# Optimization experiments

Measured on AMD Instinct MI355X. Metric: run time of the kernel, lower is better.

## Reference

```python
import jax, jax.numpy as jnp
import numpy as np

N_W, N_E, N_NUC, D_H = 8192, 32, 8, 32


def _init_linear(k, fan_in, fan_out):
    k1, k2 = jax.random.split(k)
    bound = 1.0 / np.sqrt(fan_in)
    W = jax.random.uniform(k1, (fan_in, fan_out), jnp.float32, -bound, bound)
    b = jax.random.uniform(k2, (fan_out,), jnp.float32, -bound, bound)
    return W, b


def setup_inputs() -> dict:
    key = jax.random.key(0)
    ks = jax.random.split(key, 12)
    W1_en, b1_en = _init_linear(ks[4], N_NUC, D_H)
    W2_en, b2_en = _init_linear(ks[5], D_H, D_H)
    W3_en, b3_en = _init_linear(ks[6], D_H, 1)
    W1_ee, b1_ee = _init_linear(ks[7], 1, D_H)
    W2_ee, b2_ee = _init_linear(ks[8], D_H, D_H)
    W3_ee, b3_ee = _init_linear(ks[9], D_H, 1)
    return {
        "r_electrons": jax.random.normal(ks[0], (N_W, N_E, 3), jnp.float32),
        "r_nuclei": jax.random.normal(ks[1], (N_NUC, 3), jnp.float32),
        "charges": jax.random.uniform(ks[2], (N_NUC,), jnp.float32),
        "spin_mask_parallel": jax.random.randint(ks[3], (N_E, N_E), 0, 2).astype(bool),
        "b_en": jnp.ones((N_NUC,), jnp.float32),
        "b_ee": jnp.array(1.0, jnp.float32),
        "W1_en": W1_en, "b1_en": b1_en, "W2_en": W2_en, "b2_en": b2_en,
        "W3_en": W3_en, "b3_en": b3_en,
        "W1_ee": W1_ee, "b1_ee": b1_ee, "W2_ee": W2_ee, "b2_ee": b2_ee,
        "W3_ee": W3_ee, "b3_ee": b3_ee,
        "scale_en": jnp.array(0.1, jnp.float32),
        "scale_ee": jnp.array(0.1, jnp.float32),
    }


def _mlp(x, W1, b1, W2, b2, W3, b3):
    h = jax.nn.silu(x @ W1 + b1)
    h = jax.nn.silu(h @ W2 + b2)
    return h @ W3 + b3


def reference(r_electrons, r_nuclei, charges, spin_mask_parallel,
              b_en, b_ee,
              W1_en, b1_en, W2_en, b2_en, W3_en, b3_en,
              W1_ee, b1_ee, W2_ee, b2_ee, W3_ee, b3_ee,
              scale_en, scale_ee):
    # --- electron-nucleus term ---
    d_en = r_electrons[:, :, None, :] - r_nuclei[None, None, :, :]  # [W,E,Nuc,3]
    r_en = jnp.linalg.norm(d_en, axis=-1)                            # [W,E,Nuc]
    b_en_s = jax.nn.softplus(b_en)
    J_en = jnp.sum(-charges * r_en / (1.0 + b_en_s * r_en), axis=(1, 2))  # [W]
    # r^2-killed neural correction (Linear over nuclei dim)
    J_en_nn = scale_en * jnp.sum(
        _mlp(r_en ** 2, W1_en, b1_en, W2_en, b2_en, W3_en, b3_en)[..., 0], axis=1)
    # --- electron-electron term (upper-triangular pairs only) ---
    iu, ju = np.triu_indices(N_E, k=1)  # static pair index lists, P = E*(E-1)/2
    diff = r_electrons[:, iu, :] - r_electrons[:, ju, :]  # [W,P,3]
    r_ee = jnp.linalg.norm(diff, axis=-1)                  # [W,P]
    a = jnp.where(spin_mask_parallel[iu, ju], 0.25, 0.5)   # [P]
    b_ee_s = jax.nn.softplus(b_ee)
    J_ee = jnp.sum(a * r_ee / (1.0 + b_ee_s * r_ee), axis=1)  # [W]
    J_ee_nn = scale_ee * jnp.sum(
        _mlp(r_ee[..., None], W1_ee, b1_ee, W2_ee, b2_ee, W3_ee, b3_ee)[..., 0], axis=1)
    return J_en + J_en_nn + J_ee + J_ee_nn
```

## Files before the change

kernel.cpp:

```cpp
#include <hip/hip_runtime.h>

#define N_W   8192
#define N_E   32
#define N_NUC 8
#define D_H   32
#define NTAB  4096
#define TAB_INVH 256.0f
#define TAB_H    (1.0f/256.0f)
#define WPB   8

#define AUX_OFF 4096
#define AT_OFF  4112
#define W3S_OFF 4624
#define B_OFF   4656

typedef __attribute__((ext_vector_type(8)))  short bf16x8_t;
typedef __attribute__((ext_vector_type(16))) float f32x16_t;

union FragAB { bf16x8_t s; unsigned u[4]; };

__device__ __forceinline__ float fast_rcp(float x) { return __builtin_amdgcn_rcpf(x); }
__device__ __forceinline__ float silu_f(float v)   { return v * fast_rcp(1.0f + __expf(-v)); }
__device__ __forceinline__ unsigned pk_bf16(float lo, float hi) {
    unsigned r;
    asm("v_cvt_pk_bf16_f32 %0, %1, %2" : "=v"(r) : "v"(lo), "v"(hi));
    return r;
}

__global__ void build_tables(const float* __restrict__ W1ee, const float* __restrict__ b1ee,
                             const float* __restrict__ W2ee, const float* __restrict__ b2ee,
                             const float* __restrict__ W3ee, const float* __restrict__ b3ee,
                             const float* __restrict__ scale_ee,
                             const float* __restrict__ b_en, const float* __restrict__ b_ee,
                             const int* __restrict__ mask,
                             const float* __restrict__ W2en, const float* __restrict__ W3en,
                             const float* __restrict__ b3en, const float* __restrict__ scale_en,
                             float* __restrict__ ws)
{
    const int tid = threadIdx.x;
    if (blockIdx.x == 0) {
        float* aux = ws + AUX_OFF;
        if (tid < N_NUC) aux[tid] = __logf(1.0f + __expf(b_en[tid]));
        if (tid == 8)    aux[8]   = __logf(1.0f + __expf(b_ee[0]));
        if (tid == 9)    aux[9]   = 32.0f * scale_en[0] * b3en[0];
        if (tid < D_H)   ws[W3S_OFF + tid] = W3en[tid] * scale_en[0];
        float* aT = ws + AT_OFF;
#pragma unroll
        for (int q = 0; q < 2; ++q) {
            int idx = tid + q * 256;
            int e = idx >> 4, dm = idx & 15, d = dm + 1;
            int jn = (e + d) & 31;
            int a = e < jn ? e : jn, b = e < jn ? jn : e;
            float av = mask[a * N_E + b] ? 0.25f : 0.5f;
            if (d == 16) av *= 0.5f;
            aT[e * 16 + dm] = av;
        }
        unsigned* wsB = (unsigned*)(ws + B_OFF);
#pragma unroll
        for (int q = 0; q < 2; ++q) {
            int idx = tid + q * 256;
            int lane = idx >> 3, slot = idx & 7;
            int m = slot >> 2, r = slot & 3;
            int k = m * 16 + ((lane >> 5) << 3) + (r << 1);
            int j = lane & 31;
            wsB[lane * 8 + slot] = pk_bf16(W2en[k * D_H + j], W2en[(k + 1) * D_H + j]);
        }
    }
    const int j     = tid & 31;
    const int entry = blockIdx.x * 8 + (tid >> 5);
    const float r   = (float)entry * TAB_H;
    float g = b2ee[j];
#pragma unroll
    for (int k = 0; k < D_H; ++k) g += silu_f(r * W1ee[k] + b1ee[k]) * W2ee[k * D_H + j];
    float o = silu_f(g) * W3ee[j];
#pragma unroll
    for (int m = 16; m; m >>= 1) o += __shfl_xor(o, m, 32);
    if (j == 0) ws[entry] = scale_ee[0] * (o + b3ee[0]);
}

__launch_bounds__(256, 4)
__global__ void jastrow_kernel(const float* __restrict__ re, const float* __restrict__ rnuc,
                               const float* __restrict__ charges,
                               const float* __restrict__ W1, const float* __restrict__ b1,
                               const float* __restrict__ b2,
                               const float* __restrict__ ws,
                               float* __restrict__ out)
{
    const int tid  = threadIdx.x;
    const int e    = tid & 31;
    const int half = (tid >> 5) & 1;
    const int v    = tid >> 5;
    const int w    = blockIdx.x * WPB + v;
    const float* aux = ws + AUX_OFF;

    const float* cb = re + ((size_t)w * N_E + e) * 3;
    float ex = cb[0], ey = cb[1], ez = cb[2];

    float acc = 0.0f;

    float x[N_NUC];
#pragma unroll
    for (int n = 0; n < N_NUC; ++n) {
        float dx = ex - rnuc[n * 3 + 0];
        float dy = ey - rnuc[n * 3 + 1];
        float dz = ez - rnuc[n * 3 + 2];
        float r2 = dx * dx + dy * dy + dz * dz;
        x[n] = r2;
        float r = sqrtf(r2);
        acc -= charges[n] * r * fast_rcp(1.0f + aux[n] * r);
    }

    float2 hh[D_H / 2];
#pragma unroll
    for (int j = 0; j < D_H / 2; ++j) hh[j] = ((const float2*)b1)[j];
#pragma unroll
    for (int k = 0; k < N_NUC; ++k) {
        float xk = x[k];
        const float2* row = (const float2*)(W1 + k * D_H);
#pragma unroll
        for (int j = 0; j < D_H / 2; ++j) {
            float2 wv = row[j];
            hh[j].x = fmaf(xk, wv.x, hh[j].x);
            hh[j].y = fmaf(xk, wv.y, hh[j].y);
        }
    }
    unsigned hpk[16];
#pragma unroll
    for (int i = 0; i < 16; ++i) hpk[i] = pk_bf16(silu_f(hh[i].x), silu_f(hh[i].y));
    unsigned sx[16];
#pragma unroll
    for (int i = 0; i < 16; ++i) sx[i] = (unsigned)__shfl_xor((int)hpk[i], 32, 64);

    FragAB B1, B2;
    {
        const unsigned* wsB = (const unsigned*)(ws + B_OFF) + (size_t)(tid & 63) * 8;
        uint4 q0 = *(const uint4*)wsB;
        uint4 q1 = *(const uint4*)(wsB + 4);
        B1.u[0] = q0.x; B1.u[1] = q0.y; B1.u[2] = q0.z; B1.u[3] = q0.w;
        B2.u[0] = q1.x; B2.u[1] = q1.y; B2.u[2] = q1.z; B2.u[3] = q1.w;
    }
    const bool lo = (tid & 32) == 0;
    FragAB A1a, A2a, A1b, A2b;
#pragma unroll
    for (int r = 0; r < 4; ++r) {
        A1a.u[r] = lo ? hpk[r]      : sx[4 + r];
        A2a.u[r] = lo ? hpk[8 + r]  : sx[12 + r];
        A1b.u[r] = lo ? sx[r]       : hpk[4 + r];
        A2b.u[r] = lo ? sx[8 + r]   : hpk[12 + r];
    }
    float vb2 = b2[e];
    f32x16_t accA, accB;
#pragma unroll
    for (int r = 0; r < 16; ++r) { accA[r] = vb2; accB[r] = vb2; }
    accA = __builtin_amdgcn_mfma_f32_32x32x16_bf16(A1a.s, B1.s, accA, 0, 0, 0);
    accA = __builtin_amdgcn_mfma_f32_32x32x16_bf16(A2a.s, B2.s, accA, 0, 0, 0);
    accB = __builtin_amdgcn_mfma_f32_32x32x16_bf16(A1b.s, B1.s, accB, 0, 0, 0);
    accB = __builtin_amdgcn_mfma_f32_32x32x16_bf16(A2b.s, B2.s, accB, 0, 0, 0);

    float w3s = ws[W3S_OFF + e];
    float sA = 0.0f, sB = 0.0f;
#pragma unroll
    for (int r = 0; r < 16; ++r) { sA += silu_f(accA[r]); sB += silu_f(accB[r]); }
    float mlpA = sA * w3s, mlpB = sB * w3s;

    float bs = aux[8];
    float av[16];
    {
        const float* aT = ws + AT_OFF + e * 16;
#pragma unroll
        for (int i = 0; i < 16; ++i) av[i] = aT[i];
    }
#pragma unroll
    for (int d = 1; d <= 16; ++d) {
        int jn = (e + d) & 31;
        float cjx = __shfl(ex, jn, 32);
        float cjy = __shfl(ey, jn, 32);
        float cjz = __shfl(ez, jn, 32);
        float dx = ex - cjx, dy = ey - cjy, dz = ez - cjz;
        float r = sqrtf(dx * dx + dy * dy + dz * dz);
        float ct = av[d - 1] * r * fast_rcp(1.0f + bs * r);
        float t = r * TAB_INVH;
        int i0 = (int)t;
        if (i0 > NTAB - 2) i0 = NTAB - 2;
        float f = t - (float)i0;
        const float* tp = ws + i0;
        float tv = tp[0] + f * (tp[1] - tp[0]);
        acc += ct + ((d == 16) ? 0.5f * tv : tv);
    }

    float valA = mlpA + (half ? 0.0f : acc);
    float valB = mlpB + (half ? acc : 0.0f);
#pragma unroll
    for (int m = 32; m; m >>= 1) {
        valA += __shfl_xor(valA, m, 64);
        valB += __shfl_xor(valB, m, 64);
    }
    if ((tid & 63) == 0) {
        int wA = blockIdx.x * WPB + ((tid >> 6) << 1);
        out[wA]     = valA + aux[9];
        out[wA + 1] = valB + aux[9];
    }
}

extern "C" void kernel_launch(void* const* d_in, const int* in_sizes, int n_in,
                              void* d_out, int out_size, void* d_ws, size_t ws_size,
                              hipStream_t stream)
{
    const float* re       = (const float*)d_in[0];
    const float* rnuc     = (const float*)d_in[1];
    const float* charges  = (const float*)d_in[2];
    const int*   mask     = (const int*)d_in[3];
    const float* b_en     = (const float*)d_in[4];
    const float* b_ee     = (const float*)d_in[5];
    const float* W1_en    = (const float*)d_in[6];
    const float* b1_en    = (const float*)d_in[7];
    const float* W2_en    = (const float*)d_in[8];
    const float* b2_en    = (const float*)d_in[9];
    const float* W3_en    = (const float*)d_in[10];
    const float* b3_en    = (const float*)d_in[11];
    const float* W1_ee    = (const float*)d_in[12];
    const float* b1_ee    = (const float*)d_in[13];
    const float* W2_ee    = (const float*)d_in[14];
    const float* b2_ee    = (const float*)d_in[15];
    const float* W3_ee    = (const float*)d_in[16];
    const float* b3_ee    = (const float*)d_in[17];
    const float* scale_en = (const float*)d_in[18];
    const float* scale_ee = (const float*)d_in[19];

    float* out = (float*)d_out;
    float* ws  = (float*)d_ws;

    build_tables<<<NTAB / 8, 256, 0, stream>>>(W1_ee, b1_ee, W2_ee, b2_ee, W3_ee, b3_ee,
                                               scale_ee, b_en, b_ee, mask,
                                               W2_en, W3_en, b3_en, scale_en, ws);
    jastrow_kernel<<<N_W / WPB, 256, 0, stream>>>(re, rnuc, charges,
                                                  W1_en, b1_en, b2_en, ws, out);
}
```

Before: 23.49 us.

## Map one walker per wavefront, splitting MLP K-halves and pair loop across half-waves

Restructures the work mapping so each 64-lane wavefront handles a single walker instead of two. Each half-wave now computes its own K-half of the hidden activations, which removes the cross-half shuffles, and a single pair of MFMAs replaces the previous four. The electron-electron pair loop is split between the two half-waves, 8 offsets each. This halves walkers per block and raises the launch-bounds occupancy hint, trading more blocks and duplicated electron-nucleus work for shorter per-thread serial chains.

After: 83.34 us. 255% more time.

```diff
diff --git a/kernel.cpp b/kernel.cpp
--- a/kernel.cpp
+++ b/kernel.cpp
@@ -7,7 +7,7 @@
 #define NTAB  4096
 #define TAB_INVH 256.0f
 #define TAB_H    (1.0f/256.0f)
-#define WPB   8
+#define WPB   4
 
 #define AUX_OFF 4096
 #define AT_OFF  4112
@@ -78,7 +78,7 @@
     if (j == 0) ws[entry] = scale_ee[0] * (o + b3ee[0]);
 }
 
-__launch_bounds__(256, 4)
+__launch_bounds__(256, 8)
 __global__ void jastrow_kernel(const float* __restrict__ re, const float* __restrict__ rnuc,
                                const float* __restrict__ charges,
                                const float* __restrict__ W1, const float* __restrict__ b1,
@@ -86,19 +86,17 @@
                                const float* __restrict__ ws,
                                float* __restrict__ out)
 {
-    const int tid  = threadIdx.x;
-    const int e    = tid & 31;
-    const int half = (tid >> 5) & 1;
-    const int v    = tid >> 5;
-    const int w    = blockIdx.x * WPB + v;
+    const int tid = threadIdx.x;
+    const int e   = tid & 31;
+    const int kh  = (tid >> 5) & 1;
+    const int w   = blockIdx.x * WPB + (tid >> 6);
     const float* aux = ws + AUX_OFF;
 
     const float* cb = re + ((size_t)w * N_E + e) * 3;
     float ex = cb[0], ey = cb[1], ez = cb[2];
 
-    float acc = 0.0f;
-
     float x[N_NUC];
+    float cusp = 0.0f;
 #pragma unroll
     for (int n = 0; n < N_NUC; ++n) {
         float dx = ex - rnuc[n * 3 + 0];
@@ -107,8 +105,9 @@
         float r2 = dx * dx + dy * dy + dz * dz;
         x[n] = r2;
         float r = sqrtf(r2);
-        acc -= charges[n] * r * fast_rcp(1.0f + aux[n] * r);
-    }
+        cusp -= charges[n] * r * fast_rcp(1.0f + aux[n] * r);
+    }
+    float acc = 0.5f * cusp;
 
     float2 hh[D_H / 2];
 #pragma unroll
@@ -124,12 +123,14 @@
             hh[j].y = fmaf(xk, wv.y, hh[j].y);
         }
     }
-    unsigned hpk[16];
-#pragma unroll
-    for (int i = 0; i < 16; ++i) hpk[i] = pk_bf16(silu_f(hh[i].x), silu_f(hh[i].y));
-    unsigned sx[16];
-#pragma unroll
-    for (int i = 0; i < 16; ++i) sx[i] = (unsigned)__shfl_xor((int)hpk[i], 32, 64);
+    FragAB A1, A2;
+#pragma unroll
+    for (int r = 0; r < 4; ++r) {
+        float2 s1 = kh ? hh[4 + r]  : hh[r];
+        float2 s2 = kh ? hh[12 + r] : hh[8 + r];
+        A1.u[r] = pk_bf16(silu_f(s1.x), silu_f(s1.y));
+        A2.u[r] = pk_bf16(silu_f(s2.x), silu_f(s2.y));
+    }
 
     FragAB B1, B2;
     {
@@ -139,67 +140,50 @@
         B1.u[0] = q0.x; B1.u[1] = q0.y; B1.u[2] = q0.z; B1.u[3] = q0.w;
         B2.u[0] = q1.x; B2.u[1] = q1.y; B2.u[2] = q1.z; B2.u[3] = q1.w;
     }
-    const bool lo = (tid & 32) == 0;
-    FragAB A1a, A2a, A1b, A2b;
-#pragma unroll
-    for (int r = 0; r < 4; ++r) {
-        A1a.u[r] = lo ? hpk[r]      : sx[4 + r];
-        A2a.u[r] = lo ? hpk[8 + r]  : sx[12 + r];
-        A1b.u[r] = lo ? sx[r]       : hpk[4 + r];
-        A2b.u[r] = lo ? sx[8 + r]   : hpk[12 + r];
-    }
+
     float vb2 = b2[e];
-    f32x16_t accA, accB;
-#pragma unroll
-    for (int r = 0; r < 16; ++r) { accA[r] = vb2; accB[r] = vb2; }
-    accA = __builtin_amdgcn_mfma_f32_32x32x16_bf16(A1a.s, B1.s, accA, 0, 0, 0);
-    accA = __builtin_amdgcn_mfma_f32_32x32x16_bf16(A2a.s, B2.s, accA, 0, 0, 0);
-    accB = __builtin_amdgcn_mfma_f32_32x32x16_bf16(A1b.s, B1.s, accB, 0, 0, 0);
-    accB = __builtin_amdgcn_mfma_f32_32x32x16_bf16(A2b.s, B2.s, accB, 0, 0, 0);
+    f32x16_t accm;
+#pragma unroll
+    for (int r = 0; r < 16; ++r) accm[r] = vb2;
+    accm = __builtin_amdgcn_mfma_f32_32x32x16_bf16(A1.s, B1.s, accm, 0, 0, 0);
+    accm = __builtin_amdgcn_mfma_f32_32x32x16_bf16(A2.s, B2.s, accm, 0, 0, 0);
 
     float w3s = ws[W3S_OFF + e];
-    float sA = 0.0f, sB = 0.0f;
-#pragma unroll
-    for (int r = 0; r < 16; ++r) { sA += silu_f(accA[r]); sB += silu_f(accB[r]); }
-    float mlpA = sA * w3s, mlpB = sB * w3s;
+    float sA = 0.0f;
+#pragma unroll
+    for (int r = 0; r < 16; ++r) sA += silu_f(accm[r]);
+    acc += sA * w3s;
 
     float bs = aux[8];
-    float av[16];
+    float av[8];
     {
-        const float* aT = ws + AT_OFF + e * 16;
-#pragma unroll
-        for (int i = 0; i < 16; ++i) av[i] = aT[i];
-    }
-#pragma unroll
-    for (int d = 1; d <= 16; ++d) {
+        const float* aT = ws + AT_OFF + e * 16 + kh * 8;
+#pragma unroll
+        for (int i = 0; i < 8; ++i) av[i] = aT[i];
+    }
+#pragma unroll
+    for (int dd = 0; dd < 8; ++dd) {
+        int d = kh * 8 + dd + 1;
         int jn = (e + d) & 31;
         float cjx = __shfl(ex, jn, 32);
         float cjy = __shfl(ey, jn, 32);
         float cjz = __shfl(ez, jn, 32);
         float dx = ex - cjx, dy = ey - cjy, dz = ez - cjz;
         float r = sqrtf(dx * dx + dy * dy + dz * dz);
-        float ct = av[d - 1] * r * fast_rcp(1.0f + bs * r);
+        float ct = av[dd] * r * fast_rcp(1.0f + bs * r);
         float t = r * TAB_INVH;
         int i0 = (int)t;
         if (i0 > NTAB - 2) i0 = NTAB - 2;
         float f = t - (float)i0;
         const float* tp = ws + i0;
         float tv = tp[0] + f * (tp[1] - tp[0]);
-        acc += ct + ((d == 16) ? 0.5f * tv : tv);
-    }
-
-    float valA = mlpA + (half ? 0.0f : acc);
-    float valB = mlpB + (half ? acc : 0.0f);
-#pragma unroll
-    for (int m = 32; m; m >>= 1) {
-        valA += __shfl_xor(valA, m, 64);
-        valB += __shfl_xor(valB, m, 64);
-    }
-    if ((tid & 63) == 0) {
-        int wA = blockIdx.x * WPB + ((tid >> 6) << 1);
-        out[wA]     = valA + aux[9];
-        out[wA + 1] = valB + aux[9];
-    }
+        if (dd == 7) tv = kh ? 0.5f * tv : tv;
+        acc += ct + tv;
+    }
+
+#pragma unroll
+    for (int m = 32; m; m >>= 1) acc += __shfl_xor(acc, m, 64);
+    if ((tid & 63) == 0) out[w] = acc + aux[9];
 }
 
 extern "C" void kernel_launch(void* const* d_in, const int* in_sizes, int n_in,
```

## Tabulate pair Jastrow term with MLP in interleaved float4 slope table

Applied to the files above, without the earlier changes.

The electron-electron analytic term r/(1+b r) is now tabulated alongside the MLP correction, stored as float4 entries of value and slope, so each pair does one 16-byte table load and two FMAs instead of a reciprocal plus two scalar loads. The table is halved to 2048 entries at spacing 1/128 to limit footprint and build cost. Per-pair spin coefficients are packed into 16 bitmask words instead of a 512-entry float array. Linear interpolation of the rational term adds approximation error, and the coarser grid raises error in the MLP term.

New measurement: 22.71 us. 1.03x faster.

```diff
diff --git a/kernel.cpp b/kernel.cpp
--- a/kernel.cpp
+++ b/kernel.cpp
@@ -4,15 +4,15 @@
 #define N_E   32
 #define N_NUC 8
 #define D_H   32
-#define NTAB  4096
-#define TAB_INVH 256.0f
-#define TAB_H    (1.0f/256.0f)
+#define NTAB  2048
+#define TAB_INVH 128.0f
+#define TAB_H    (1.0f/128.0f)
 #define WPB   8
 
-#define AUX_OFF 4096
-#define AT_OFF  4112
-#define W3S_OFF 4624
-#define B_OFF   4656
+#define AUX_OFF  8192
+#define MSK_OFF  8208
+#define W3S_OFF  8224
+#define B_OFF    8256
 
 typedef __attribute__((ext_vector_type(8)))  short bf16x8_t;
 typedef __attribute__((ext_vector_type(16))) float f32x16_t;
@@ -44,38 +44,48 @@
         if (tid == 8)    aux[8]   = __logf(1.0f + __expf(b_ee[0]));
         if (tid == 9)    aux[9]   = 32.0f * scale_en[0] * b3en[0];
         if (tid < D_H)   ws[W3S_OFF + tid] = W3en[tid] * scale_en[0];
-        float* aT = ws + AT_OFF;
-#pragma unroll
-        for (int q = 0; q < 2; ++q) {
-            int idx = tid + q * 256;
-            int e = idx >> 4, dm = idx & 15, d = dm + 1;
-            int jn = (e + d) & 31;
-            int a = e < jn ? e : jn, b = e < jn ? jn : e;
-            float av = mask[a * N_E + b] ? 0.25f : 0.5f;
-            if (d == 16) av *= 0.5f;
-            aT[e * 16 + dm] = av;
+        if (tid < 16) {
+            unsigned m = 0;
+            int d = tid + 1;
+            for (int e = 0; e < N_E; ++e) {
+                int jn = (e + d) & 31;
+                int a = e < jn ? e : jn, b = e < jn ? jn : e;
+                if (mask[a * N_E + b]) m |= (1u << e);
+            }
+            ((unsigned*)(ws + MSK_OFF))[tid] = m;
         }
         unsigned* wsB = (unsigned*)(ws + B_OFF);
 #pragma unroll
         for (int q = 0; q < 2; ++q) {
             int idx = tid + q * 256;
             int lane = idx >> 3, slot = idx & 7;
-            int m = slot >> 2, r = slot & 3;
-            int k = m * 16 + ((lane >> 5) << 3) + (r << 1);
+            int m2 = slot >> 2, r = slot & 3;
+            int k = m2 * 16 + ((lane >> 5) << 3) + (r << 1);
             int j = lane & 31;
             wsB[lane * 8 + slot] = pk_bf16(W2en[k * D_H + j], W2en[(k + 1) * D_H + j]);
         }
     }
     const int j     = tid & 31;
     const int entry = blockIdx.x * 8 + (tid >> 5);
-    const float r   = (float)entry * TAB_H;
-    float g = b2ee[j];
-#pragma unroll
-    for (int k = 0; k < D_H; ++k) g += silu_f(r * W1ee[k] + b1ee[k]) * W2ee[k * D_H + j];
-    float o = silu_f(g) * W3ee[j];
-#pragma unroll
-    for (int m = 16; m; m >>= 1) o += __shfl_xor(o, m, 32);
-    if (j == 0) ws[entry] = scale_ee[0] * (o + b3ee[0]);
+    const float bs  = __logf(1.0f + __expf(b_ee[0]));
+    float mlp[2];
+#pragma unroll
+    for (int t = 0; t < 2; ++t) {
+        float r = ((float)entry + (float)t) * TAB_H;
+        float g = b2ee[j];
+#pragma unroll
+        for (int k = 0; k < D_H; ++k) g += silu_f(r * W1ee[k] + b1ee[k]) * W2ee[k * D_H + j];
+        float o = silu_f(g) * W3ee[j];
+#pragma unroll
+        for (int m = 16; m; m >>= 1) o += __shfl_xor(o, m, 32);
+        mlp[t] = scale_ee[0] * (o + b3ee[0]);
+    }
+    if (j == 0) {
+        float r0 = (float)entry * TAB_H, r1 = r0 + TAB_H;
+        float c0 = r0 * fast_rcp(1.0f + bs * r0);
+        float c1 = r1 * fast_rcp(1.0f + bs * r1);
+        *(float4*)(ws + 4 * entry) = make_float4(c0, c1 - c0, mlp[0], mlp[1] - mlp[0]);
+    }
 }
 
 __launch_bounds__(256, 4)
@@ -163,12 +173,11 @@
     for (int r = 0; r < 16; ++r) { sA += silu_f(accA[r]); sB += silu_f(accB[r]); }
     float mlpA = sA * w3s, mlpB = sB * w3s;
 
-    float bs = aux[8];
-    float av[16];
+    unsigned mks[16];
     {
-        const float* aT = ws + AT_OFF + e * 16;
-#pragma unroll
-        for (int i = 0; i < 16; ++i) av[i] = aT[i];
+        const unsigned* mp = (const unsigned*)(ws + MSK_OFF);
+#pragma unroll
+        for (int i = 0; i < 16; ++i) mks[i] = mp[i];
     }
 #pragma unroll
     for (int d = 1; d <= 16; ++d) {
@@ -178,14 +187,14 @@
         float cjz = __shfl(ez, jn, 32);
         float dx = ex - cjx, dy = ey - cjy, dz = ez - cjz;
         float r = sqrtf(dx * dx + dy * dy + dz * dz);
-        float ct = av[d - 1] * r * fast_rcp(1.0f + bs * r);
         float t = r * TAB_INVH;
         int i0 = (int)t;
         if (i0 > NTAB - 2) i0 = NTAB - 2;
         float f = t - (float)i0;
-        const float* tp = ws + i0;
-        float tv = tp[0] + f * (tp[1] - tp[0]);
-        acc += ct + ((d == 16) ? 0.5f * tv : tv);
+        float4 T = *(const float4*)(ws + 4 * i0);
+        float a = ((mks[d - 1] >> e) & 1u) ? 0.25f : 0.5f;
+        float pv = a * fmaf(f, T.y, T.x) + fmaf(f, T.w, T.z);
+        acc += (d == 16) ? 0.5f * pv : pv;
     }
 
     float valA = mlpA + (half ? 0.0f : acc);
```
